# Kernel optimization log

Measured on AMD Instinct MI355X. Metric: run time of the kernel, lower is better.

## Reference

```python
import jax, jax.numpy as jnp
import numpy as np

NH, NKV, HD = 16, 4, 128
ROPE_THETA = 10000.0


def setup_inputs() -> dict:
    key = jax.random.key(0)
    ks = jax.random.split(key, 5)
    std = jnp.float32(0.02)
    return {
        "hidden_states": jax.random.normal(ks[0], (1, 2048, 2048), jnp.float32),
        "wq": jax.random.normal(ks[1], (2048, NH * HD), jnp.float32) * std,
        "wk": jax.random.normal(ks[2], (2048, NKV * HD), jnp.float32) * std,
        "wv": jax.random.normal(ks[3], (2048, NKV * HD), jnp.float32) * std,
        "wo": jax.random.normal(ks[4], (NH * HD, 2048), jnp.float32) * std,
    }


def _rope(x, cos, sin):
    # x: [B,S,n,hd]; pairs (even,odd) treated as complex, multiplied by cis(angle)
    xr = x.reshape(*x.shape[:-1], HD // 2, 2)
    re, im = xr[..., 0], xr[..., 1]
    c = cos[None, :, None, :]  # [1,S,1,hd/2]
    s = sin[None, :, None, :]
    out = jnp.stack((re * c - im * s, re * s + im * c), axis=-1)
    return out.reshape(x.shape)


def reference(hidden_states, wq, wk, wv, wo):
    B, S, H = hidden_states.shape
    q = (hidden_states @ wq).reshape(B, S, NH, HD)
    k = (hidden_states @ wk).reshape(B, S, NKV, HD)
    v = (hidden_states @ wv).reshape(B, S, NKV, HD)

    # precompute_freqs_cis (full rotary dim, rot_dim=None)
    freqs = 1.0 / (ROPE_THETA ** (jnp.arange(0, HD, 2, dtype=jnp.float32) / HD))
    ang = jnp.outer(jnp.arange(S, dtype=jnp.float32), freqs)  # [S, hd/2]
    cos, sin = jnp.cos(ang), jnp.sin(ang)

    q = _rope(q.astype(jnp.float32), cos, sin)
    k = _rope(k.astype(jnp.float32), cos, sin)

    # GQA: repeat_kv == repeat_interleave over head axis
    n_rep = NH // NKV
    k = jnp.repeat(k, n_rep, axis=2)  # [B,S,NH,HD]
    v = jnp.repeat(v, n_rep, axis=2)

    scale = jnp.float32(1.0 / np.sqrt(HD))
    scores = jnp.einsum("bqhd,bkhd->bhqk", q, k) * scale
    causal = jnp.tril(jnp.ones((S, S), dtype=bool))
    scores = jnp.where(causal[None, None], scores, jnp.float32(-1e9))
    attn = jax.nn.softmax(scores, axis=-1)
    out = jnp.einsum("bhqk,bkhd->bqhd", attn, v).reshape(B, S, NH * HD)
    return out @ wo
```

## Files before the change

kernel.cpp:

```cpp
#include <hip/hip_runtime.h>
#include <cstdint>

typedef __attribute__((ext_vector_type(8))) short short8;
typedef __attribute__((ext_vector_type(4))) float f32x4;

static __device__ __forceinline__ unsigned short f2bf(float x) {
  union { float f; unsigned int u; } c; c.f = x;
  unsigned int u = c.u;
  unsigned int r = (u + 0x7fffu + ((u >> 16) & 1u)) >> 16;
  return (unsigned short)r;
}

static __device__ __forceinline__ void gl_lds16(const void* g, void* l) {
  __builtin_amdgcn_global_load_lds((const __attribute__((address_space(1))) void*)g,
                                   (__attribute__((address_space(3))) void*)l, 16, 0, 0);
}

__global__ __launch_bounds__(256) void k_sincos(float2* __restrict__ ctab) {
  int idx = blockIdx.x * 256 + threadIdx.x;
  int s = idx >> 6, i = idx & 63;
  float freq = powf(10000.0f, -(float)i / 64.0f);
  float sn, cs;
  sincosf((float)s * freq, &sn, &cs);
  ctab[idx] = make_float2(cs, sn);
}

__global__ __launch_bounds__(256) void k_f32_to_bf16(const float* __restrict__ src,
                                                     unsigned short* __restrict__ dst,
                                                     int n4) {
  int i = blockIdx.x * 256 + threadIdx.x;
  if (i >= n4) return;
  float4 v = reinterpret_cast<const float4*>(src)[i];
  ushort4 o;
  o.x = f2bf(v.x); o.y = f2bf(v.y); o.z = f2bf(v.z); o.w = f2bf(v.w);
  reinterpret_cast<ushort4*>(dst)[i] = o;
}

__global__ __launch_bounds__(256) void k_transpose_all(const float* __restrict__ wq,
                                                       const float* __restrict__ wk,
                                                       const float* __restrict__ wv,
                                                       const float* __restrict__ wo,
                                                       unsigned short* __restrict__ wqt,
                                                       unsigned short* __restrict__ wkt,
                                                       unsigned short* __restrict__ wvt,
                                                       unsigned short* __restrict__ wot) {
  __shared__ float tile[32][33];
  int id = blockIdx.x;
  const float* src; unsigned short* dst; int N, t;
  if (id < 4096)       { src = wq; dst = wqt; N = 2048; t = id; }
  else if (id < 8192)  { src = wo; dst = wot; N = 2048; t = id - 4096; }
  else if (id < 9216)  { src = wk; dst = wkt; N = 512;  t = id - 8192; }
  else                 { src = wv; dst = wvt; N = 512;  t = id - 9216; }
  const int K = 2048;
  int ntx = N >> 5;
  int bn = (t % ntx) * 32, bk = (t / ntx) * 32;
  int tx = threadIdx.x & 31, ty = threadIdx.x >> 5;
#pragma unroll
  for (int i = 0; i < 32; i += 8)
    tile[ty + i][tx] = src[(size_t)(bk + ty + i) * N + bn + tx];
  __syncthreads();
#pragma unroll
  for (int i = 0; i < 32; i += 8)
    dst[(size_t)(bn + ty + i) * K + bk + tx] = f2bf(tile[tx][ty + i]);
}

__global__ __launch_bounds__(256) void k_gemm_bf16(const unsigned short* __restrict__ A,
                                                   const unsigned short* __restrict__ Bt,
                                                   float* __restrict__ C,
                                                   unsigned short* __restrict__ Qd,
                                                   unsigned short* __restrict__ Kd,
                                                   unsigned short* __restrict__ VT,
                                                   const float2* __restrict__ ctab,
                                                   int M, int N, int K, int fuse) {
  __shared__ short sA[2][128 * 64];
  __shared__ short sB[2][64 * 64];
  int tid = threadIdx.x;
  int lane = tid & 63, wid = tid >> 6;
  int wr = wid >> 1, wc = wid & 1;

  int gx = gridDim.x, nwg = gx * gridDim.y;
  int flat = blockIdx.y * gx + blockIdx.x;
  int l = (flat & 7) * (nwg >> 3) + (flat >> 3);
  int bx = l % gx, by = l / gx;
  int m0 = by * 128, n0 = bx * 64;

  f32x4 acc[4][2] = {};

  int srcCol = (((tid & 7) ^ ((tid >> 3) & 7)) << 3);
  int rA = tid >> 3;
  const unsigned short* Ag = A + (size_t)(m0 + rA) * K + srcCol;
  const unsigned short* Bg = Bt + (size_t)(n0 + rA) * K + srcCol;
  int wb = (tid & ~63) * 8;

  int g = lane >> 4, fr = lane & 15, sw = fr & 7;

#define STAGE_G(buf, kof) do { \
    gl_lds16(Ag + (kof),                    &sA[buf][wb]); \
    gl_lds16(Ag + 32 * (size_t)K + (kof),   &sA[buf][2048 + wb]); \
    gl_lds16(Ag + 64 * (size_t)K + (kof),   &sA[buf][4096 + wb]); \
    gl_lds16(Ag + 96 * (size_t)K + (kof),   &sA[buf][6144 + wb]); \
    gl_lds16(Bg + (kof),                    &sB[buf][wb]); \
    gl_lds16(Bg + 32 * (size_t)K + (kof),   &sB[buf][2048 + wb]); \
  } while (0)

  int nt = K >> 6;
  STAGE_G(0, 0);
  __syncthreads();

  int cur = 0;
  for (int t = 0; t < nt; t++) {
    if (t + 1 < nt) STAGE_G(cur ^ 1, (size_t)((t + 1) << 6));
    const short* sAc = sA[cur];
    const short* sBc = sB[cur];
#pragma unroll
    for (int kk = 0; kk < 2; kk++) {
      int so = ((((kk << 2) + g) ^ sw) << 3);
      short8 af[4], bf2[2];
#pragma unroll
      for (int x = 0; x < 4; x++)
        af[x] = *(const short8*)(sAc + (wr * 64 + x * 16 + fr) * 64 + so);
#pragma unroll
      for (int ni = 0; ni < 2; ni++)
        bf2[ni] = *(const short8*)(sBc + (wc * 32 + ni * 16 + fr) * 64 + so);
#pragma unroll
      for (int x = 0; x < 4; x++)
#pragma unroll
        for (int ni = 0; ni < 2; ni++)
          acc[x][ni] = __builtin_amdgcn_mfma_f32_16x16x32_bf16(af[x], bf2[ni], acc[x][ni], 0, 0, 0);
    }
    __syncthreads();
    cur ^= 1;
  }
#undef STAGE_G

  int rb = m0 + wr * 64 + (g << 2);
  if (!fuse) {
#pragma unroll
    for (int ni = 0; ni < 2; ni++) {
      int col = n0 + wc * 32 + ni * 16 + fr;
#pragma unroll
      for (int x = 0; x < 4; x++)
#pragma unroll
        for (int j = 0; j < 4; j++)
          C[(size_t)(rb + x * 16 + j) * N + col] = acc[x][ni][j];
    }
    return;
  }

  const float QAMP = 0.12751742836257666f;
#pragma unroll
  for (int ni = 0; ni < 2; ni++) {
    int col = n0 + wc * 32 + ni * 16 + fr;
    if (col >= 2560) {
#pragma unroll
      for (int x = 0; x < 4; x++) {
        ushort4 pk;
        pk.x = f2bf(acc[x][ni][0]); pk.y = f2bf(acc[x][ni][1]);
        pk.z = f2bf(acc[x][ni][2]); pk.w = f2bf(acc[x][ni][3]);
        *(ushort4*)(VT + (size_t)(col - 2560) * 2048 + rb + x * 16) = pk;
      }
    } else {
      int ipair = (col & 127) >> 1;
      bool even = (col & 1) == 0;
      bool isQ = col < 2048;
      unsigned short* dst = isQ ? Qd : Kd;
      int stride = isQ ? 2048 : 512;
      int dcol = isQ ? col : (col - 2048);
      float amp = isQ ? QAMP : 1.0f;
#pragma unroll
      for (int x = 0; x < 4; x++) {
        f32x4 a = acc[x][ni];
        float p0 = __shfl_xor(a[0], 1), p1 = __shfl_xor(a[1], 1);
        float p2 = __shfl_xor(a[2], 1), p3 = __shfl_xor(a[3], 1);
        float pv[4] = {p0, p1, p2, p3};
#pragma unroll
        for (int j = 0; j < 4; j++) {
          int r = rb + x * 16 + j;
          float2 cs = ctab[r * 64 + ipair];
          float o = even ? (a[j] * cs.x - pv[j] * cs.y)
                         : (pv[j] * cs.y + a[j] * cs.x);
          dst[(size_t)r * stride + dcol] = f2bf(o * amp);
        }
      }
    }
  }
}

#define KSTR 136
#define VSTR 72
#define PSTR 72
__global__ __launch_bounds__(256) void k_attn_mfma(const unsigned short* __restrict__ Qb,
                                                   const unsigned short* __restrict__ Kb,
                                                   const unsigned short* __restrict__ Vt,
                                                   unsigned short* __restrict__ O) {
  __shared__ short sK[2][64 * KSTR];
  __shared__ short sV[2][128 * VSTR];
  __shared__ short sP[4][16 * PSTR];
  int h = blockIdx.y;
  int x = blockIdx.x;
  int qb = (h < 8) ? x : (31 - x);
  int q0 = qb * 64;
  int kvh = h >> 2;
  int tid = threadIdx.x, lane = tid & 63, w = tid >> 6;
  int fr = lane & 15, g = lane >> 4, kq = g << 3;

  short8 qf[4];
  {
    const unsigned short* qrow = Qb + (size_t)(q0 + w * 16 + fr) * 2048 + h * 128 + kq;
#pragma unroll
    for (int ko = 0; ko < 4; ko++) qf[ko] = *(const short8*)(qrow + ko * 32);
  }

  f32x4 oacc[8];
#pragma unroll
  for (int nd = 0; nd < 8; nd++) oacc[nd] = (f32x4){0.f, 0.f, 0.f, 0.f};
  float m_i = -3e38f;
  float l_i = 0.f;

  int skr = tid >> 2, skc = (tid & 3) << 5;
  int svd = tid >> 1, svc = (tid & 1) << 5;
  const unsigned short* Kbase = Kb + (size_t)kvh * 128 + skc;
  const unsigned short* Vbase = Vt + (size_t)(kvh * 128 + svd) * 2048 + svc;
  short* pw = (short*)sP[w];
  int kdOff = skr * KSTR + skc;
  int vdOff = svd * VSTR + svc;

  short8 kreg[4], vreg[4];
  {
    const short8* ks = (const short8*)(Kbase + (size_t)skr * 512);
    const short8* vs = (const short8*)(Vbase);
#pragma unroll
    for (int j = 0; j < 4; j++) { kreg[j] = ks[j]; vreg[j] = vs[j]; }
  }
  {
    short* kd = sK[0] + kdOff; short* vd = sV[0] + vdOff;
#pragma unroll
    for (int j = 0; j < 4; j++) { *(short8*)(kd + j * 8) = kreg[j]; *(short8*)(vd + j * 8) = vreg[j]; }
  }
  if (qb >= 1) {
    const short8* ks = (const short8*)(Kbase + (size_t)(64 + skr) * 512);
    const short8* vs = (const short8*)(Vbase + 64);
#pragma unroll
    for (int j = 0; j < 4; j++) { kreg[j] = ks[j]; vreg[j] = vs[j]; }
  }
  __syncthreads();

  int qrowS = q0 + w * 16 + fr;

  for (int kt = 0; kt <= qb; kt++) {
    int c = kt & 1;
    const short* sKc = sK[c];
    const short* sVc = sV[c];

    f32x4 sacc[4];
#pragma unroll
    for (int ni = 0; ni < 4; ni++) sacc[ni] = (f32x4){0.f, 0.f, 0.f, 0.f};
    __builtin_amdgcn_s_setprio(1);
#pragma unroll
    for (int ko = 0; ko < 4; ko++)
#pragma unroll
      for (int ni = 0; ni < 4; ni++) {
        short8 kf = *(const short8*)(sKc + (ni * 16 + fr) * KSTR + kq + ko * 32);
        sacc[ni] = __builtin_amdgcn_mfma_f32_16x16x32_bf16(kf, qf[ko], sacc[ni], 0, 0, 0);
      }
    __builtin_amdgcn_s_setprio(0);

    if (kt == qb) {
      int k0 = kt * 64;
#pragma unroll
      for (int ni = 0; ni < 4; ni++) {
        int kc = k0 + ni * 16 + (g << 2);
#pragma unroll
        for (int j = 0; j < 4; j++)
          if (kc + j > qrowS) sacc[ni][j] = -3e38f;
      }
    }

    float tm = sacc[0][0];
#pragma unroll
    for (int ni = 0; ni < 4; ni++)
#pragma unroll
      for (int j = 0; j < 4; j++) tm = fmaxf(tm, sacc[ni][j]);
    tm = fmaxf(tm, __shfl_xor(tm, 16));
    tm = fmaxf(tm, __shfl_xor(tm, 32));

    if (!__all(tm <= m_i + 8.0f)) {
      float mn = fmaxf(m_i, tm);
      float sc = exp2f(m_i - mn);
      m_i = mn;
      float scj[4];
#pragma unroll
      for (int j = 0; j < 4; j++) scj[j] = __shfl(sc, (g << 2) + j);
#pragma unroll
      for (int nd = 0; nd < 8; nd++)
#pragma unroll
        for (int j = 0; j < 4; j++) oacc[nd][j] *= scj[j];
      l_i *= sc;
    }

    float ps = 0.f;
#pragma unroll
    for (int ni = 0; ni < 4; ni++) {
      float p0 = exp2f(sacc[ni][0] - m_i);
      float p1 = exp2f(sacc[ni][1] - m_i);
      float p2 = exp2f(sacc[ni][2] - m_i);
      float p3 = exp2f(sacc[ni][3] - m_i);
      ps += (p0 + p1) + (p2 + p3);
      ushort4 pk;
      pk.x = f2bf(p0); pk.y = f2bf(p1); pk.z = f2bf(p2); pk.w = f2bf(p3);
      *(ushort4*)(pw + fr * PSTR + ni * 16 + (g << 2)) = pk;
    }
    ps += __shfl_xor(ps, 16);
    ps += __shfl_xor(ps, 32);
    l_i += ps;

    __builtin_amdgcn_s_setprio(1);
#pragma unroll
    for (int ks = 0; ks < 2; ks++) {
      short8 pa = *(const short8*)(pw + fr * PSTR + kq + ks * 32);
#pragma unroll
      for (int nd = 0; nd < 8; nd++) {
        short8 vb = *(const short8*)(sVc + (nd * 16 + fr) * VSTR + kq + ks * 32);
        oacc[nd] = __builtin_amdgcn_mfma_f32_16x16x32_bf16(pa, vb, oacc[nd], 0, 0, 0);
      }
    }
    __builtin_amdgcn_s_setprio(0);

    if (kt < qb) {
      short* kd = sK[c ^ 1] + kdOff; short* vd = sV[c ^ 1] + vdOff;
#pragma unroll
      for (int j = 0; j < 4; j++) { *(short8*)(kd + j * 8) = kreg[j]; *(short8*)(vd + j * 8) = vreg[j]; }
      if (kt + 1 < qb) {
        int k2 = (kt + 2) * 64;
        const short8* ks = (const short8*)(Kbase + (size_t)(k2 + skr) * 512);
        const short8* vs = (const short8*)(Vbase + k2);
#pragma unroll
        for (int j = 0; j < 4; j++) { kreg[j] = ks[j]; vreg[j] = vs[j]; }
      }
      __syncthreads();
    }
  }

  int orow = q0 + w * 16 + (g << 2);
#pragma unroll
  for (int j = 0; j < 4; j++) {
    float lj = __shfl(l_i, (g << 2) + j);
    float inv = 1.0f / lj;
#pragma unroll
    for (int nd = 0; nd < 8; nd++)
      O[(size_t)(orow + j) * 2048 + h * 128 + nd * 16 + fr] = f2bf(oacc[nd][j] * inv);
  }
}

extern "C" void kernel_launch(void* const* d_in, const int* in_sizes, int n_in,
                              void* d_out, int out_size, void* d_ws, size_t ws_size,
                              hipStream_t stream) {
  const float* hs = (const float*)d_in[0];
  const float* wq = (const float*)d_in[1];
  const float* wk = (const float*)d_in[2];
  const float* wv = (const float*)d_in[3];
  const float* wo = (const float*)d_in[4];
  char* ws = (char*)d_ws;

  unsigned short* hb   = (unsigned short*)(ws);
  unsigned short* wqt  = (unsigned short*)(ws + 8388608);
  unsigned short* wkt  = (unsigned short*)(ws + 16777216);
  unsigned short* wvt  = (unsigned short*)(ws + 18874368);
  unsigned short* wot  = (unsigned short*)(ws + 20971520);
  unsigned short* q_bf = (unsigned short*)(ws + 29360128);
  unsigned short* k_bf = (unsigned short*)(ws + 37748736);
  unsigned short* vt_bf= (unsigned short*)(ws + 39845888);
  float2* ctab         = (float2*)(ws + 41943040);
  unsigned short* ao   = hb;
  float* out = (float*)d_out;

  k_sincos<<<512, 256, 0, stream>>>(ctab);
  k_f32_to_bf16<<<4096, 256, 0, stream>>>(hs, hb, 2048 * 2048 / 4);
  k_transpose_all<<<10240, 256, 0, stream>>>(wq, wk, wv, wo, wqt, wkt, wvt, wot);

  k_gemm_bf16<<<dim3(48, 16), 256, 0, stream>>>(hb, wqt, (float*)nullptr,
                                                q_bf, k_bf, vt_bf, ctab,
                                                2048, 3072, 2048, 1);

  k_attn_mfma<<<dim3(32, 16), 256, 0, stream>>>(q_bf, k_bf, vt_bf, ao);

  k_gemm_bf16<<<dim3(32, 16), 256, 0, stream>>>(ao, wot, out,
                                                (unsigned short*)nullptr,
                                                (unsigned short*)nullptr,
                                                (unsigned short*)nullptr,
                                                (const float2*)nullptr,
                                                2048, 2048, 2048, 0);
}
```

Before: 147.0 us.

## Split long causal attention query blocks across KV halves with combine kernel

The attention kernel now splits the upper 16 query blocks into two KV-range halves (split-K/flash-decoding style), launching 48 blocks per head instead of 32 to balance causal work across more workgroups. Partial unnormalized outputs and running max/sum are written to reused workspace, and a new combine kernel merges them with log-sum-exp weighting. This adds an extra kernel launch, extra global traffic and bf16 rounding of partial outputs in exchange for better load balance and occupancy.

```diff
diff --git a/kernel.cpp b/kernel.cpp
--- a/kernel.cpp
+++ b/kernel.cpp
@@ -9,6 +9,11 @@
   unsigned int u = c.u;
   unsigned int r = (u + 0x7fffu + ((u >> 16) & 1u)) >> 16;
   return (unsigned short)r;
+}
+
+static __device__ __forceinline__ float bf2f(unsigned short x) {
+  union { unsigned int u; float f; } c; c.u = ((unsigned int)x) << 16;
+  return c.f;
 }
 
 static __device__ __forceinline__ void gl_lds16(const void* g, void* l) {
@@ -192,13 +197,27 @@
 __global__ __launch_bounds__(256) void k_attn_mfma(const unsigned short* __restrict__ Qb,
                                                    const unsigned short* __restrict__ Kb,
                                                    const unsigned short* __restrict__ Vt,
-                                                   unsigned short* __restrict__ O) {
+                                                   unsigned short* __restrict__ O,
+                                                   unsigned short* __restrict__ pO,
+                                                   float* __restrict__ pML) {
   __shared__ short sK[2][64 * KSTR];
   __shared__ short sV[2][128 * VSTR];
   __shared__ short sP[4][16 * PSTR];
   int h = blockIdx.y;
-  int x = blockIdx.x;
-  int qb = (h < 8) ? x : (31 - x);
+  int k3 = blockIdx.x / 3, r3 = blockIdx.x % 3;
+  int item = (r3 == 0) ? (15 - k3) : ((r3 == 1) ? (47 - 2 * k3) : (46 - 2 * k3));
+  int qb, ks, ke, half, mode;
+  if (item < 16) {
+    qb = item; ks = 0; ke = qb + 1; half = 0; mode = 0;
+  } else {
+    int i2 = item - 16;
+    qb = 16 + (i2 >> 1);
+    half = i2 & 1;
+    int nh = (qb + 1) >> 1;
+    ks = half ? nh : 0;
+    ke = half ? (qb + 1) : nh;
+    mode = 1;
+  }
   int q0 = qb * 64;
   int kvh = h >> 2;
   int tid = threadIdx.x, lane = tid & 63, w = tid >> 6;
@@ -227,28 +246,28 @@
 
   short8 kreg[4], vreg[4];
   {
-    const short8* ks = (const short8*)(Kbase + (size_t)skr * 512);
-    const short8* vs = (const short8*)(Vbase);
-#pragma unroll
-    for (int j = 0; j < 4; j++) { kreg[j] = ks[j]; vreg[j] = vs[j]; }
+    const short8* ksrc = (const short8*)(Kbase + (size_t)(ks * 64 + skr) * 512);
+    const short8* vsrc = (const short8*)(Vbase + ks * 64);
+#pragma unroll
+    for (int j = 0; j < 4; j++) { kreg[j] = ksrc[j]; vreg[j] = vsrc[j]; }
   }
   {
     short* kd = sK[0] + kdOff; short* vd = sV[0] + vdOff;
 #pragma unroll
     for (int j = 0; j < 4; j++) { *(short8*)(kd + j * 8) = kreg[j]; *(short8*)(vd + j * 8) = vreg[j]; }
   }
-  if (qb >= 1) {
-    const short8* ks = (const short8*)(Kbase + (size_t)(64 + skr) * 512);
-    const short8* vs = (const short8*)(Vbase + 64);
-#pragma unroll
-    for (int j = 0; j < 4; j++) { kreg[j] = ks[j]; vreg[j] = vs[j]; }
+  if (ke - ks >= 2) {
+    const short8* ksrc = (const short8*)(Kbase + (size_t)((ks + 1) * 64 + skr) * 512);
+    const short8* vsrc = (const short8*)(Vbase + (ks + 1) * 64);
+#pragma unroll
+    for (int j = 0; j < 4; j++) { kreg[j] = ksrc[j]; vreg[j] = vsrc[j]; }
   }
   __syncthreads();
 
   int qrowS = q0 + w * 16 + fr;
 
-  for (int kt = 0; kt <= qb; kt++) {
-    int c = kt & 1;
+  for (int kt = ks; kt < ke; kt++) {
+    int c = (kt - ks) & 1;
     const short* sKc = sK[c];
     const short* sVc = sV[c];
 
@@ -316,40 +335,74 @@
 
     __builtin_amdgcn_s_setprio(1);
 #pragma unroll
-    for (int ks = 0; ks < 2; ks++) {
-      short8 pa = *(const short8*)(pw + fr * PSTR + kq + ks * 32);
+    for (int ksl = 0; ksl < 2; ksl++) {
+      short8 pa = *(const short8*)(pw + fr * PSTR + kq + ksl * 32);
 #pragma unroll
       for (int nd = 0; nd < 8; nd++) {
-        short8 vb = *(const short8*)(sVc + (nd * 16 + fr) * VSTR + kq + ks * 32);
+        short8 vb = *(const short8*)(sVc + (nd * 16 + fr) * VSTR + kq + ksl * 32);
         oacc[nd] = __builtin_amdgcn_mfma_f32_16x16x32_bf16(pa, vb, oacc[nd], 0, 0, 0);
       }
     }
     __builtin_amdgcn_s_setprio(0);
 
-    if (kt < qb) {
+    if (kt + 1 < ke) {
       short* kd = sK[c ^ 1] + kdOff; short* vd = sV[c ^ 1] + vdOff;
 #pragma unroll
       for (int j = 0; j < 4; j++) { *(short8*)(kd + j * 8) = kreg[j]; *(short8*)(vd + j * 8) = vreg[j]; }
-      if (kt + 1 < qb) {
+      if (kt + 2 < ke) {
         int k2 = (kt + 2) * 64;
-        const short8* ks = (const short8*)(Kbase + (size_t)(k2 + skr) * 512);
-        const short8* vs = (const short8*)(Vbase + k2);
-#pragma unroll
-        for (int j = 0; j < 4; j++) { kreg[j] = ks[j]; vreg[j] = vs[j]; }
+        const short8* ksrc = (const short8*)(Kbase + (size_t)(k2 + skr) * 512);
+        const short8* vsrc = (const short8*)(Vbase + k2);
+#pragma unroll
+        for (int j = 0; j < 4; j++) { kreg[j] = ksrc[j]; vreg[j] = vsrc[j]; }
       }
       __syncthreads();
     }
   }
 
-  int orow = q0 + w * 16 + (g << 2);
-#pragma unroll
-  for (int j = 0; j < 4; j++) {
-    float lj = __shfl(l_i, (g << 2) + j);
-    float inv = 1.0f / lj;
-#pragma unroll
-    for (int nd = 0; nd < 8; nd++)
-      O[(size_t)(orow + j) * 2048 + h * 128 + nd * 16 + fr] = f2bf(oacc[nd][j] * inv);
-  }
+  if (mode == 0) {
+    int orow = q0 + w * 16 + (g << 2);
+#pragma unroll
+    for (int j = 0; j < 4; j++) {
+      float lj = __shfl(l_i, (g << 2) + j);
+      float inv = 1.0f / lj;
+#pragma unroll
+      for (int nd = 0; nd < 8; nd++)
+        O[(size_t)(orow + j) * 2048 + h * 128 + nd * 16 + fr] = f2bf(oacc[nd][j] * inv);
+    }
+  } else {
+    size_t base = ((size_t)(h * 16 + (qb - 16)) * 2 + half) * 64;
+    int rl0 = w * 16 + (g << 2);
+#pragma unroll
+    for (int j = 0; j < 4; j++)
+#pragma unroll
+      for (int nd = 0; nd < 8; nd++)
+        pO[(base + rl0 + j) * 128 + nd * 16 + fr] = f2bf(oacc[nd][j]);
+    if (g == 0) {
+      size_t r = base + w * 16 + fr;
+      pML[r * 2] = m_i;
+      pML[r * 2 + 1] = l_i;
+    }
+  }
+}
+
+__global__ __launch_bounds__(256) void k_combine(const unsigned short* __restrict__ pO,
+                                                 const float* __restrict__ pML,
+                                                 unsigned short* __restrict__ O) {
+  int t = blockIdx.x * 256 + threadIdx.x;
+  int col = t & 127;
+  int rg = t >> 7;
+  int h = rg >> 10, rl = rg & 1023;
+  size_t r0 = ((size_t)(h * 16 + (rl >> 6)) * 2 + 0) * 64 + (rl & 63);
+  size_t r1 = ((size_t)(h * 16 + (rl >> 6)) * 2 + 1) * 64 + (rl & 63);
+  float m0 = pML[r0 * 2], l0 = pML[r0 * 2 + 1];
+  float m1 = pML[r1 * 2], l1 = pML[r1 * 2 + 1];
+  float M = fmaxf(m0, m1);
+  float w0 = exp2f(m0 - M), w1 = exp2f(m1 - M);
+  float inv = 1.0f / (w0 * l0 + w1 * l1);
+  float o0 = bf2f(pO[r0 * 128 + col]);
+  float o1 = bf2f(pO[r1 * 128 + col]);
+  O[(size_t)(1024 + rl) * 2048 + h * 128 + col] = f2bf((w0 * o0 + w1 * o1) * inv);
 }
 
 extern "C" void kernel_launch(void* const* d_in, const int* in_sizes, int n_in,
@@ -372,6 +425,8 @@
   unsigned short* vt_bf= (unsigned short*)(ws + 39845888);
   float2* ctab         = (float2*)(ws + 41943040);
   unsigned short* ao   = hb;
+  unsigned short* pO   = wqt;
+  float* pML           = (float*)wkt;
   float* out = (float*)d_out;
 
   k_sincos<<<512, 256, 0, stream>>>(ctab);
@@ -382,7 +437,8 @@
                                                 q_bf, k_bf, vt_bf, ctab,
                                                 2048, 3072, 2048, 1);
 
-  k_attn_mfma<<<dim3(32, 16), 256, 0, stream>>>(q_bf, k_bf, vt_bf, ao);
+  k_attn_mfma<<<dim3(48, 16), 256, 0, stream>>>(q_bf, k_bf, vt_bf, ao, pO, pML);
+  k_combine<<<8192, 256, 0, stream>>>(pO, pML, ao);
 
   k_gemm_bf16<<<dim3(32, 16), 256, 0, stream>>>(ao, wot, out,
                                                 (unsigned short*)nullptr,
```

Result: slower. 156.5 us (+6.4%).

## Software-pipeline QK^T so next tile's scores overlap current softmax

Applied to the files above, without the earlier changes.

The attention loop now computes the scores for the first key tile before the loop. Each iteration then stages the next K/V tile into shared memory and issues the QK^T MFMAs for that next tile before running softmax and PV on the current one. The goal is to let the matrix units work while the exp and reduction ALU work is in flight, hiding the dependency between the score MFMAs and softmax. In exchange it adds a second __syncthreads per iteration and keeps an extra set of score accumulators live, which raises register pressure.

```diff
diff --git a/kernel.cpp b/kernel.cpp
--- a/kernel.cpp
+++ b/kernel.cpp
@@ -245,25 +245,51 @@
   }
   __syncthreads();
 
+  f32x4 scur[4];
+#pragma unroll
+  for (int ni = 0; ni < 4; ni++) scur[ni] = (f32x4){0.f, 0.f, 0.f, 0.f};
+  __builtin_amdgcn_s_setprio(1);
+#pragma unroll
+  for (int ko = 0; ko < 4; ko++)
+#pragma unroll
+    for (int ni = 0; ni < 4; ni++) {
+      short8 kf = *(const short8*)(sK[0] + (ni * 16 + fr) * KSTR + kq + ko * 32);
+      scur[ni] = __builtin_amdgcn_mfma_f32_16x16x32_bf16(kf, qf[ko], scur[ni], 0, 0, 0);
+    }
+  __builtin_amdgcn_s_setprio(0);
+
   int qrowS = q0 + w * 16 + fr;
 
   for (int kt = 0; kt <= qb; kt++) {
     int c = kt & 1;
-    const short* sKc = sK[c];
-    const short* sVc = sV[c];
-
-    f32x4 sacc[4];
-#pragma unroll
-    for (int ni = 0; ni < 4; ni++) sacc[ni] = (f32x4){0.f, 0.f, 0.f, 0.f};
-    __builtin_amdgcn_s_setprio(1);
-#pragma unroll
-    for (int ko = 0; ko < 4; ko++)
-#pragma unroll
-      for (int ni = 0; ni < 4; ni++) {
-        short8 kf = *(const short8*)(sKc + (ni * 16 + fr) * KSTR + kq + ko * 32);
-        sacc[ni] = __builtin_amdgcn_mfma_f32_16x16x32_bf16(kf, qf[ko], sacc[ni], 0, 0, 0);
+    f32x4 snx[4];
+#pragma unroll
+    for (int ni = 0; ni < 4; ni++) snx[ni] = (f32x4){0.f, 0.f, 0.f, 0.f};
+
+    if (kt < qb) {
+      __syncthreads();
+      short* kd = sK[c ^ 1] + kdOff; short* vd = sV[c ^ 1] + vdOff;
+#pragma unroll
+      for (int j = 0; j < 4; j++) { *(short8*)(kd + j * 8) = kreg[j]; *(short8*)(vd + j * 8) = vreg[j]; }
+      if (kt + 1 < qb) {
+        int k2 = (kt + 2) * 64;
+        const short8* ks = (const short8*)(Kbase + (size_t)(k2 + skr) * 512);
+        const short8* vs = (const short8*)(Vbase + k2);
+#pragma unroll
+        for (int j = 0; j < 4; j++) { kreg[j] = ks[j]; vreg[j] = vs[j]; }
       }
-    __builtin_amdgcn_s_setprio(0);
+      __syncthreads();
+      const short* sKn = sK[c ^ 1];
+      __builtin_amdgcn_s_setprio(1);
+#pragma unroll
+      for (int ko = 0; ko < 4; ko++)
+#pragma unroll
+        for (int ni = 0; ni < 4; ni++) {
+          short8 kf = *(const short8*)(sKn + (ni * 16 + fr) * KSTR + kq + ko * 32);
+          snx[ni] = __builtin_amdgcn_mfma_f32_16x16x32_bf16(kf, qf[ko], snx[ni], 0, 0, 0);
+        }
+      __builtin_amdgcn_s_setprio(0);
+    }
 
     if (kt == qb) {
       int k0 = kt * 64;
@@ -272,15 +298,15 @@
         int kc = k0 + ni * 16 + (g << 2);
 #pragma unroll
         for (int j = 0; j < 4; j++)
-          if (kc + j > qrowS) sacc[ni][j] = -3e38f;
+          if (kc + j > qrowS) scur[ni][j] = -3e38f;
       }
     }
 
-    float tm = sacc[0][0];
+    float tm = scur[0][0];
 #pragma unroll
     for (int ni = 0; ni < 4; ni++)
 #pragma unroll
-      for (int j = 0; j < 4; j++) tm = fmaxf(tm, sacc[ni][j]);
+      for (int j = 0; j < 4; j++) tm = fmaxf(tm, scur[ni][j]);
     tm = fmaxf(tm, __shfl_xor(tm, 16));
     tm = fmaxf(tm, __shfl_xor(tm, 32));
 
@@ -301,10 +327,10 @@
     float ps = 0.f;
 #pragma unroll
     for (int ni = 0; ni < 4; ni++) {
-      float p0 = exp2f(sacc[ni][0] - m_i);
-      float p1 = exp2f(sacc[ni][1] - m_i);
-      float p2 = exp2f(sacc[ni][2] - m_i);
-      float p3 = exp2f(sacc[ni][3] - m_i);
+      float p0 = exp2f(scur[ni][0] - m_i);
+      float p1 = exp2f(scur[ni][1] - m_i);
+      float p2 = exp2f(scur[ni][2] - m_i);
+      float p3 = exp2f(scur[ni][3] - m_i);
       ps += (p0 + p1) + (p2 + p3);
       ushort4 pk;
       pk.x = f2bf(p0); pk.y = f2bf(p1); pk.z = f2bf(p2); pk.w = f2bf(p3);
@@ -314,6 +340,7 @@
     ps += __shfl_xor(ps, 32);
     l_i += ps;
 
+    const short* sVc = sV[c];
     __builtin_amdgcn_s_setprio(1);
 #pragma unroll
     for (int ks = 0; ks < 2; ks++) {
@@ -327,17 +354,8 @@
     __builtin_amdgcn_s_setprio(0);
 
     if (kt < qb) {
-      short* kd = sK[c ^ 1] + kdOff; short* vd = sV[c ^ 1] + vdOff;
-#pragma unroll
-      for (int j = 0; j < 4; j++) { *(short8*)(kd + j * 8) = kreg[j]; *(short8*)(vd + j * 8) = vreg[j]; }
-      if (kt + 1 < qb) {
-        int k2 = (kt + 2) * 64;
-        const short8* ks = (const short8*)(Kbase + (size_t)(k2 + skr) * 512);
-        const short8* vs = (const short8*)(Vbase + k2);
-#pragma unroll
-        for (int j = 0; j < 4; j++) { kreg[j] = ks[j]; vreg[j] = vs[j]; }
-      }
-      __syncthreads();
+#pragma unroll
+      for (int ni = 0; ni < 4; ni++) scur[ni] = snx[ni];
     }
   }
 
```

Result: slower. 150.2 us (+2.2%).
